# Kernel optimization log

Measured on AMD Instinct MI355X. Metric: run time of the kernel, lower is better.

Reference implementation:

```python
import jax, jax.numpy as jnp
import numpy as np
import math

B, T, C = 2, 1024, 1024
H = 16
HS = C // H          # head size 64
ROT = HS // 2        # rotary dims 32
TT = 1024            # ctx_len
FFN = 4 * C
EPS = 1e-6


def _layernorm(x, g, b):
    m = jnp.mean(x, -1, keepdims=True)
    v = jnp.mean((x - m) ** 2, -1, keepdims=True)
    return (x - m) * jax.lax.rsqrt(v + EPS) * g + b


def _time_shift_half(x):
    # ZeroPad2d((0,0,1,-1)) applied to first half of channels: shift by one step in time
    c = x.shape[-1]
    a = jnp.pad(x[:, :, : c // 2], ((0, 0), (1, 0), (0, 0)))[:, :-1, :]
    return jnp.concatenate([a, x[:, :, c // 2 :]], axis=-1)


def _rotate_half(x):
    x1, x2 = jnp.split(x, 2, axis=-1)
    return jnp.concatenate([-x2, x1], axis=-1)


def _rotary_cos_sin(t_len, rot, base):
    inv_freq = 1.0 / (base ** (jnp.arange(0, rot, 2, dtype=jnp.float32) / rot))
    freqs = jnp.arange(t_len, dtype=jnp.float32)[:, None] * inv_freq[None, :]
    emb = jnp.concatenate([freqs, freqs], axis=-1)  # (T, rot)
    return jnp.cos(emb), jnp.sin(emb)


def _build_w(time_w, time_alpha, time_beta, t_len):
    # faithful translation of the pad/tile/reshape circulant trick
    w = jnp.pad(time_w, ((0, 0), (0, TT)))            # (H, 2TT)
    w = jnp.tile(w, (1, TT))                          # (H, 2TT*TT)
    w = w[:, :-TT].reshape(-1, TT, 2 * TT - 1)        # (H, TT, 2TT-1)
    w = w[:, :, TT - 1 :]                             # (H, TT, TT)
    return w[:, :t_len, :t_len] * time_alpha[:, :, :t_len] * time_beta[:, :t_len, :]


def setup_inputs() -> dict:
    key = jax.random.key(0)
    ks = jax.random.split(key, 24)
    s = 0.02
    d = {
        "x": jax.random.normal(ks[0], (B, T, C), jnp.float32),
        "ln1_g": jnp.ones((C,), jnp.float32),
        "ln1_b": jnp.zeros((C,), jnp.float32),
        "Wq": jax.random.normal(ks[1], (C, C), jnp.float32) * s,
        "bq": jnp.zeros((C,), jnp.float32),
        "Wk": jax.random.normal(ks[2], (C, C), jnp.float32) * s,
        "bk": jnp.zeros((C,), jnp.float32),
        "Wv": jax.random.normal(ks[3], (C, C), jnp.float32) * s,
        "bv": jnp.zeros((C,), jnp.float32),
        "Wo": jax.random.normal(ks[4], (C, C), jnp.float32) * s,
        "bo": jnp.zeros((C,), jnp.float32),
        "time_w": 1.0 + 0.01 * jax.random.normal(ks[5], (H, TT), jnp.float32),
        "time_alpha": 1.0 + 0.01 * jax.random.normal(ks[6], (H, 1, TT), jnp.float32),
        "time_beta": 1.0 + 0.01 * jax.random.normal(ks[7], (H, TT, 1), jnp.float32),
        "time_gamma": 1.0 + 0.01 * jax.random.normal(ks[8], (TT, 1), jnp.float32),
        "Wmix": jnp.eye(H, dtype=jnp.float32) + 0.01 * jax.random.normal(ks[9], (H, H), jnp.float32),
        "ln2_g": jnp.ones((C,), jnp.float32),
        "ln2_b": jnp.zeros((C,), jnp.float32),
        "Wgk": jax.random.normal(ks[10], (C, FFN), jnp.float32) * s,
        "bgk": jnp.zeros((FFN,), jnp.float32),
        "Wgv": jax.random.normal(ks[11], (C, FFN), jnp.float32) * s,
        "bgv": jnp.zeros((FFN,), jnp.float32),
        "Wgw": jax.random.normal(ks[12], (FFN, C), jnp.float32) * s,
        "bgw": jnp.zeros((C,), jnp.float32),
    }
    return d


def _block(x, ln1_g, ln1_b, Wq, bq, Wk, bk, Wv, bv, Wo, bo,
           time_w, time_alpha, time_beta, time_gamma, Wmix,
           ln2_g, ln2_b, Wgk, bgk, Wgv, bgv, Wgw, bgw):
    b, t, c = x.shape
    # ---- MHA_pro attention sublayer (pre-LN residual) ----
    xs = _time_shift_half(_layernorm(x, ln1_g, ln1_b))
    q = (xs @ Wq + bq).reshape(b, t, H, HS).transpose(0, 2, 1, 3)  # bhtd
    k = (xs @ Wk + bk).reshape(b, t, H, HS).transpose(0, 2, 1, 3)
    v = (xs @ Wv + bv).reshape(b, t, H, HS).transpose(0, 2, 1, 3)
    qr, qp = q[..., :ROT], q[..., ROT:]
    kr, kp = k[..., :ROT], k[..., ROT:]
    cos, sin = _rotary_cos_sin(t, ROT, float(TT))  # base = ctx_len
    qr = qr * cos + _rotate_half(qr) * sin
    kr = kr * cos + _rotate_half(kr) * sin
    q = jnp.concatenate([qr, qp], axis=-1)
    k = jnp.concatenate([kr, kp], axis=-1)
    att = jnp.einsum("bhtd,bhud->bhtu", q, k) * (1.0 / math.sqrt(HS))
    causal = jnp.tril(jnp.ones((t, t), bool))
    att = jnp.where(causal, att, -jnp.inf)
    att = jax.nn.softmax(att, axis=-1)
    w = _build_w(time_w, time_alpha, time_beta, t)  # (H, T, T)
    att = att * w[None]
    att = jnp.einsum("ij,bjtu->bitu", Wmix, att)  # 1x1 conv head mix
    y = jnp.einsum("bhtu,bhud->bhtd", att, v)
    y = y.transpose(0, 2, 1, 3).reshape(b, t, c)
    y = (y @ Wo + bo) * time_gamma[:t, :]
    x = x + y
    # ---- GeGLU MLP sublayer (pre-LN residual) ----
    xm = _layernorm(x, ln2_g, ln2_b)
    kk = xm @ Wgk + bgk
    vv = xm @ Wgv + bgv
    y2 = (jax.nn.gelu(kk, approximate=False) * vv) @ Wgw + bgw
    return x + y2


def reference(x, ln1_g, ln1_b, Wq, bq, Wk, bk, Wv, bv, Wo, bo,
              time_w, time_alpha, time_beta, time_gamma, Wmix,
              ln2_g, ln2_b, Wgk, bgk, Wgv, bgv, Wgw, bgw):
    return _block(x, ln1_g, ln1_b, Wq, bq, Wk, bk, Wv, bv, Wo, bo,
                  time_w, time_alpha, time_beta, time_gamma, Wmix,
                  ln2_g, ln2_b, Wgk, bgk, Wgv, bgv, Wgw, bgw)
```

## Files before the change

### kernel.cpp

```cpp
#include <hip/hip_runtime.h>
#include <math.h>

typedef unsigned short u16;
typedef short s16x8 __attribute__((ext_vector_type(8)));
typedef float f32x4 __attribute__((ext_vector_type(4)));

#define TB 2
#define TSEQ 1024
#define CC 1024
#define NH 16
#define HSZ 64
#define FFN 4096
#define MROWS (TB*TSEQ)

#define GLOAD16(g, l) __builtin_amdgcn_global_load_lds( \
    (const __attribute__((address_space(1))) unsigned*)(g), \
    (__attribute__((address_space(3))) unsigned*)(l), 16, 0, 0)

#define SBAR()  __builtin_amdgcn_s_barrier()
#define SCHED0() __builtin_amdgcn_sched_barrier(0)
#define LGKM0() asm volatile("s_waitcnt lgkmcnt(0)" ::: "memory")
#define WAITV4() asm volatile("s_waitcnt vmcnt(4)" ::: "memory")
#define PRIO(n) __builtin_amdgcn_s_setprio(n)

__device__ __forceinline__ float bf2f(u16 u){
  union { unsigned u; float f; } c; c.u = ((unsigned)u) << 16; return c.f;
}
__device__ __forceinline__ u16 f2bf(float f){
  union { float f; unsigned u; } c; c.f = f;
  unsigned u = c.u;
  u += 0x7fffu + ((u >> 16) & 1);
  return (u16)(u >> 16);
}
__device__ __forceinline__ float ldin(const void* p, size_t i, int bf){
  return bf ? bf2f(((const u16*)p)[i]) : ((const float*)p)[i];
}

__global__ void k_flag(const unsigned* __restrict__ g, int* __restrict__ flag){
  if (threadIdx.x == 0) *flag = (g[0] == 0x3F800000u) ? 0 : 1;
}

__global__ void k_transpose_cvt(const void* __restrict__ in, u16* __restrict__ out,
                                int R, int Cc, const int* __restrict__ flagp){
  int bf = *flagp;
  __shared__ u16 tile[32][33];
  int bx = blockIdx.x * 32, by = blockIdx.y * 32;
  int tx = threadIdx.x & 31, ty = threadIdx.x >> 5;
  #pragma unroll
  for (int i = 0; i < 32; i += 8)
    tile[ty + i][tx] = f2bf(ldin(in, (size_t)(by + ty + i) * Cc + bx + tx, bf));
  __syncthreads();
  #pragma unroll
  for (int i = 0; i < 32; i += 8)
    out[(size_t)(bx + ty + i) * R + by + tx] = tile[tx][ty + i];
}

__global__ void k_cvt(const void* __restrict__ in, u16* __restrict__ out, int n,
                      const int* __restrict__ flagp){
  int bf = *flagp;
  int i = blockIdx.x * 256 + threadIdx.x;
  if (i < n) out[i] = f2bf(ldin(in, i, bf));
}

__global__ void k_tw8(const void* __restrict__ tw, u16* __restrict__ tw8,
                      const int* __restrict__ flagp){
  int bf = *flagp;
  int idx = blockIdx.x*256 + threadIdx.x;
  int s = idx >> 14;
  int h = (idx >> 10) & 15;
  int k = idx & 1023;
  float v = (k + s < 1024) ? ldin(tw, h*1024 + k + s, bf) : 0.f;
  tw8[idx] = f2bf(v);
}

__global__ void k_ln1_shift(const void* __restrict__ x, const void* __restrict__ g,
                            const void* __restrict__ bta, u16* __restrict__ xs,
                            const int* __restrict__ flagp){
  int bf = *flagp;
  int row = blockIdx.x;
  int t = row & (TSEQ - 1);
  int tid = threadIdx.x;
  float v[4]; float s = 0.f, ss = 0.f;
  #pragma unroll
  for (int i = 0; i < 4; i++){
    v[i] = ldin(x, (size_t)row * CC + tid*4 + i, bf);
    s += v[i]; ss += v[i]*v[i];
  }
  __shared__ float rs[256], rss[256];
  rs[tid] = s; rss[tid] = ss; __syncthreads();
  for (int o = 128; o > 0; o >>= 1){ if (tid < o){ rs[tid] += rs[tid+o]; rss[tid] += rss[tid+o]; } __syncthreads(); }
  float mean = rs[0] * (1.0f/CC);
  float var  = rss[0] * (1.0f/CC) - mean*mean;
  float inv  = rsqrtf(var + 1e-6f);
  #pragma unroll
  for (int i = 0; i < 4; i++){
    int c = tid*4 + i;
    float o = (v[i]-mean)*inv*ldin(g, c, bf) + ldin(bta, c, bf);
    u16 ob = f2bf(o);
    if (c >= CC/2)            xs[(size_t)row*CC + c] = ob;
    else if (t < TSEQ-1)      xs[(size_t)(row+1)*CC + c] = ob;
  }
  if (t == 0 && tid < 128){
    #pragma unroll
    for (int i = 0; i < 4; i++) xs[(size_t)row*CC + tid*4 + i] = 0;
  }
}

__global__ void k_ln2(const float* __restrict__ x1, const void* __restrict__ g,
                      const void* __restrict__ bta, u16* __restrict__ xm,
                      const int* __restrict__ flagp){
  int bf = *flagp;
  int row = blockIdx.x;
  int tid = threadIdx.x;
  const float* xr = x1 + (size_t)row * CC;
  float v[4]; float s = 0.f, ss = 0.f;
  #pragma unroll
  for (int i = 0; i < 4; i++){ v[i] = xr[tid*4 + i]; s += v[i]; ss += v[i]*v[i]; }
  __shared__ float rs[256], rss[256];
  rs[tid] = s; rss[tid] = ss; __syncthreads();
  for (int o = 128; o > 0; o >>= 1){ if (tid < o){ rs[tid] += rs[tid+o]; rss[tid] += rss[tid+o]; } __syncthreads(); }
  float mean = rs[0] * (1.0f/CC);
  float var  = rss[0] * (1.0f/CC) - mean*mean;
  float inv  = rsqrtf(var + 1e-6f);
  #pragma unroll
  for (int i = 0; i < 4; i++){
    int c = tid*4 + i;
    xm[(size_t)row*CC + c] = f2bf((v[i]-mean)*inv*ldin(g, c, bf) + ldin(bta, c, bf));
  }
}

__global__ void k_rotary(u16* __restrict__ qkv){
  int idx = blockIdx.x*256 + threadIdx.x;
  int i = idx & 15;
  int h = (idx >> 4) & (NH-1);
  int row = idx >> 8;
  int t = row & (TSEQ-1);
  float invf = exp2f(-0.625f * (float)i);
  float ang = (float)t * invf;
  float cs = cosf(ang), sn = sinf(ang);
  size_t base = (size_t)row * (3*CC);
  u16* qp = qkv + base + h*HSZ;
  float a = bf2f(qp[i]), b2 = bf2f(qp[i+16]);
  qp[i]    = f2bf(a*cs - b2*sn);
  qp[i+16] = f2bf(b2*cs + a*sn);
  u16* kp = qkv + base + CC + h*HSZ;
  a = bf2f(kp[i]); b2 = bf2f(kp[i+16]);
  kp[i]    = f2bf(a*cs - b2*sn);
  kp[i+16] = f2bf(b2*cs + a*sn);
}

__global__ __launch_bounds__(256) void k_qk(
    const u16* __restrict__ qkv, u16* __restrict__ att)
{
  int m0 = blockIdx.y * 128;
  int n0 = blockIdx.x * 128;
  if (n0 > m0) return;
  int bh = blockIdx.z; int b = bh >> 4, h = bh & 15;
  __shared__ u16 As[128*32];
  __shared__ u16 Bs[128*32];
  int tid = threadIdx.x;
  int w = tid >> 6;
  int lane = tid & 63;
  int wm = (w >> 1) * 64, wn = (w & 1) * 64;
  f32x4 acc[4][4];
  #pragma unroll
  for (int i = 0; i < 4; i++)
    #pragma unroll
    for (int j = 0; j < 4; j++) acc[i][j] = (f32x4){0.f,0.f,0.f,0.f};

  int rr = lane >> 2;
  int cc = lane & 3;
  const u16* gA0 = qkv + (size_t)(b*TSEQ + m0 + w*32 + rr)*(3*CC) + h*HSZ + cc*8;
  const u16* gA1 = gA0 + (size_t)16*(3*CC);
  const u16* gB0 = qkv + (size_t)(b*TSEQ + n0 + w*32 + rr)*(3*CC) + CC + h*HSZ + cc*8;
  const u16* gB1 = gB0 + (size_t)16*(3*CC);
  u16* lA0 = As + (w*32)*32;
  u16* lA1 = As + (w*32+16)*32;
  u16* lB0 = Bs + (w*32)*32;
  u16* lB1 = Bs + (w*32+16)*32;
  int quad = lane >> 4;
  int l15 = lane & 15;

  #pragma unroll
  for (int k0 = 0; k0 < HSZ; k0 += 32){
    __syncthreads();
    GLOAD16(gA0 + k0, lA0);
    GLOAD16(gA1 + k0, lA1);
    GLOAD16(gB0 + k0, lB0);
    GLOAD16(gB1 + k0, lB1);
    __syncthreads();
    s16x8 af[4], bfr[4];
    #pragma unroll
    for (int i = 0; i < 4; i++){
      af[i]  = *(s16x8*)&As[(wm + i*16 + l15)*32 + quad*8];
      bfr[i] = *(s16x8*)&Bs[(wn + i*16 + l15)*32 + quad*8];
    }
    #pragma unroll
    for (int mi = 0; mi < 4; mi++)
      #pragma unroll
      for (int ni = 0; ni < 4; ni++)
        acc[mi][ni] = __builtin_amdgcn_mfma_f32_16x16x32_bf16(af[mi], bfr[ni], acc[mi][ni], 0, 0, 0);
  }

  #pragma unroll
  for (int mi = 0; mi < 4; mi++){
    int rowb = m0 + wm + mi*16 + quad*4;
    #pragma unroll
    for (int ni = 0; ni < 4; ni++){
      int col = n0 + wn + ni*16 + l15;
      #pragma unroll
      for (int r = 0; r < 4; r++){
        int t = rowb + r;
        att[((size_t)bh*TSEQ + t)*TSEQ + col] = f2bf(acc[mi][ni][r] * 0.125f);
      }
    }
  }
}

__global__ __launch_bounds__(256) void k_softmix(
    u16* __restrict__ att, const u16* __restrict__ tw8, const u16* __restrict__ al16,
    const u16* __restrict__ be16, const void* __restrict__ wmix,
    const int* __restrict__ flagp)
{
  int bf = *flagp;
  int bt = blockIdx.x;
  int t = bt & (TSEQ-1);
  int b = bt >> 10;
  int tid = threadIdx.x;
  int wv = tid >> 6;
  int lane = tid & 63;
  int tile_end = ((t >> 7) + 1) << 7;
  int nchunk = (t >> 9) + 1;
  int sh = (TSEQ-1 - t) & 7;
  int base = (TSEQ-1 - t) - sh;
  __shared__ __align__(16) u16 P[NH][TSEQ];
  __shared__ float wm[NH*NH];
  if (tid < NH*NH) wm[tid] = ldin(wmix, tid, bf);

  #pragma unroll
  for (int hi = 0; hi < 4; hi++){
    int h = wv*4 + hi;
    const u16* srow = att + ((size_t)(b*NH + h)*TSEQ + t)*TSEQ;
    const u16* twp  = tw8 + ((size_t)sh*NH + h)*TSEQ + base;
    const u16* alp  = al16 + h*TSEQ;
    float v[16];
    float lmax = -1e30f;
    for (int r = 0; r < nchunk; r++){
      int ub = lane*8 + r*512;
      uint4 pk = *(const uint4*)(srow + ub);
      const u16* pe = (const u16*)&pk;
      #pragma unroll
      for (int e = 0; e < 8; e++){
        float s = bf2f(pe[e]);
        if (ub + e > t) s = -1e30f;
        v[r*8+e] = s;
        lmax = fmaxf(lmax, s);
      }
    }
    #pragma unroll
    for (int o = 32; o > 0; o >>= 1) lmax = fmaxf(lmax, __shfl_xor(lmax, o));
    float lsum = 0.f;
    for (int r = 0; r < nchunk; r++){
      #pragma unroll
      for (int e = 0; e < 8; e++){
        float p = __expf(v[r*8+e] - lmax);
        v[r*8+e] = p; lsum += p;
      }
    }
    #pragma unroll
    for (int o = 32; o > 0; o >>= 1) lsum += __shfl_xor(lsum, o);
    float btv = bf2f(be16[h*TSEQ + t]);
    float inv = btv / lsum;
    for (int r = 0; r < nchunk; r++){
      int ub = lane*8 + r*512;
      uint4 wk = *(const uint4*)(twp + ub);
      uint4 ak = *(const uint4*)(alp + ub);
      const u16* we = (const u16*)&wk;
      const u16* ae = (const u16*)&ak;
      u16 tmp[8];
      #pragma unroll
      for (int e = 0; e < 8; e++){
        float p = v[r*8+e] * inv * bf2f(we[e]) * bf2f(ae[e]);
        tmp[e] = f2bf(p);
      }
      *(uint4*)&P[h][ub] = *(uint4*)tmp;
    }
  }
  __syncthreads();

  int u0 = tid * 4;
  if (u0 < tile_end){
    #pragma unroll
    for (int half2 = 0; half2 < 2; half2++){
      float acc[8][4];
      #pragma unroll
      for (int i = 0; i < 8; i++)
        #pragma unroll
        for (int k = 0; k < 4; k++) acc[i][k] = 0.f;
      #pragma unroll
      for (int j = 0; j < 16; j++){
        uint2 pk = *(const uint2*)&P[j][u0];
        float p0 = bf2f((u16)(pk.x & 0xffff)), p1 = bf2f((u16)(pk.x >> 16));
        float p2 = bf2f((u16)(pk.y & 0xffff)), p3 = bf2f((u16)(pk.y >> 16));
        #pragma unroll
        for (int i2 = 0; i2 < 8; i2++){
          float w = wm[(half2*8 + i2)*NH + j];
          acc[i2][0] += w*p0; acc[i2][1] += w*p1; acc[i2][2] += w*p2; acc[i2][3] += w*p3;
        }
      }
      #pragma unroll
      for (int i2 = 0; i2 < 8; i2++){
        int i = half2*8 + i2;
        u16 tmp[4] = {f2bf(acc[i2][0]), f2bf(acc[i2][1]), f2bf(acc[i2][2]), f2bf(acc[i2][3])};
        *(uint2*)(att + ((size_t)(b*NH + i)*TSEQ + t)*TSEQ + u0) = *(uint2*)tmp;
      }
    }
  }
}

__global__ void k_vt(const u16* __restrict__ qkv, u16* __restrict__ vt){
  __shared__ u16 tile[32][33];
  int bh = blockIdx.z; int b = bh >> 4, h = bh & 15;
  int u0 = blockIdx.x * 32, d0 = blockIdx.y * 32;
  int tx = threadIdx.x & 31, ty = threadIdx.x >> 5;
  #pragma unroll
  for (int i = 0; i < 32; i += 8)
    tile[ty + i][tx] = qkv[(size_t)(b*TSEQ + u0 + ty + i)*(3*CC) + 2*CC + h*HSZ + d0 + tx];
  __syncthreads();
  #pragma unroll
  for (int i = 0; i < 32; i += 8)
    vt[((size_t)bh*HSZ + d0 + ty + i)*TSEQ + u0 + tx] = tile[tx][ty + i];
}

__global__ void k_gelumul(const u16* __restrict__ kkvv, u16* __restrict__ hh){
  int idx = blockIdx.x*256 + threadIdx.x;
  int m = idx >> 9;
  int j = (idx & 511) * 8;
  uint4 kk4 = *(const uint4*)(kkvv + (size_t)m*(2*FFN) + j);
  uint4 vv4 = *(const uint4*)(kkvv + (size_t)m*(2*FFN) + FFN + j);
  const u16* ks = (const u16*)&kk4;
  const u16* vs = (const u16*)&vv4;
  u16 out[8];
  #pragma unroll
  for (int e = 0; e < 8; e++){
    float kk = bf2f(ks[e]), vv = bf2f(vs[e]);
    float ge = 0.5f*kk*(1.0f + erff(kk*0.70710678f));
    out[e] = f2bf(ge*vv);
  }
  *(uint4*)(hh + (size_t)m*FFN + j) = *(uint4*)out;
}

__global__ __launch_bounds__(512, 2) void k_gemm256(
    const u16* __restrict__ A, const u16* __restrict__ Bt,
    const u16* __restrict__ bias, int M, int N, int K, int mode,
    u16* __restrict__ outp, float* __restrict__ partial)
{
  __shared__ u16 S[65536];
  u16* SA0 = S;
  u16* SB0 = S + 16384;
  u16* SA1 = S + 32768;
  u16* SB1 = S + 49152;

  int nwg = (int)(gridDim.x * gridDim.y * gridDim.z);
  int lin = (int)(blockIdx.x + gridDim.x * (blockIdx.y + gridDim.y * blockIdx.z));
  int nl  = (nwg & 7) ? lin : ((lin & 7) * (nwg >> 3) + (lin >> 3));
  int bx  = nl % (int)gridDim.x;
  int tq  = nl / (int)gridDim.x;
  int by  = tq % (int)gridDim.y;
  int bz  = tq / (int)gridDim.y;

  int m0 = by * 256, n0 = bx * 256;
  int kper = K / (int)gridDim.z;
  int kbeg = bz * kper;
  int nt = kper >> 6;
  int niter = nt >> 1;

  int tid = threadIdx.x;
  int w = tid >> 6, lane = tid & 63;
  int wm = w >> 2, wn = w & 3;
  int quad = lane >> 4, l15 = lane & 15;
  int l3 = lane >> 3, ch = (lane & 7) ^ l3;

  const u16* gA = A  + (size_t)(m0 + w*16 + l3) * K + ch*8 + kbeg;
  const u16* gB = Bt + (size_t)(n0 + w*16 + l3) * K + ch*8 + kbeg;
  const size_t hstep = (size_t)128 * K;
  const size_t rstep = (size_t)8 * K;

  int pc0 = quad ^ (l15 & 7);
  int pc1 = (4 + quad) ^ (l15 & 7);
  int aoff0 = (wm*128 + l15)*64 + pc0*8;
  int aoff1 = (wm*128 + l15)*64 + pc1*8;
  int boff0 = (wn*64 + l15)*64 + pc0*8;
  int boff1 = (wn*64 + l15)*64 + pc1*8;

  f32x4 acc[8][4];
  #pragma unroll
  for (int i = 0; i < 8; i++)
    #pragma unroll
    for (int j = 0; j < 4; j++) acc[i][j] = (f32x4){0.f,0.f,0.f,0.f};

  #define STG(gbase, sbase, h, ko) do{ \
      const u16* _g = (gbase) + (size_t)(h)*hstep + (ko); \
      u16* _l = (sbase) + ((h)*128 + w*16)*64; \
      GLOAD16(_g, _l); \
      GLOAD16(_g + rstep, _l + 512); \
    }while(0)

  #define LD_A(buf, MQ) do{ _Pragma("unroll") for (int _m = 0; _m < 4; _m++){ \
      a0[_m] = *(const s16x8*)((buf) + aoff0 + (MQ)*4096 + _m*1024); \
      a1[_m] = *(const s16x8*)((buf) + aoff1 + (MQ)*4096 + _m*1024); } }while(0)

  #define LD_B(buf, NQ, B0A, B1A) do{ _Pragma("unroll") for (int _n = 0; _n < 2; _n++){ \
      B0A[_n] = *(const s16x8*)((buf) + boff0 + (NQ)*2048 + _n*1024); \
      B1A[_n] = *(const s16x8*)((buf) + boff1 + (NQ)*2048 + _n*1024); } }while(0)

  #define MMQ(MQ, NQ, B0A, B1A) do{ _Pragma("unroll") for (int _m = 0; _m < 4; _m++){ \
      _Pragma("unroll") for (int _n = 0; _n < 2; _n++){ \
        acc[(MQ)*4+_m][(NQ)*2+_n] = __builtin_amdgcn_mfma_f32_16x16x32_bf16(a0[_m], B0A[_n], acc[(MQ)*4+_m][(NQ)*2+_n], 0, 0, 0); \
        acc[(MQ)*4+_m][(NQ)*2+_n] = __builtin_amdgcn_mfma_f32_16x16x32_bf16(a1[_m], B1A[_n], acc[(MQ)*4+_m][(NQ)*2+_n], 0, 0, 0); }} }while(0)

  STG(gB, SB0, 0, 0); STG(gB, SB0, 1, 0);
  STG(gA, SA0, 0, 0); STG(gA, SA0, 1, 0);
  STG(gB, SB1, 0, 64); STG(gB, SB1, 1, 64);
  WAITV4();
  SBAR();

  s16x8 a0[4], a1[4], bl0[2], bl1[2], bh0[2], bh1[2];

  for (int i = 0; i < niter; i++){
    int t1k = (2*i+1)*64;
    int t2k = (2*i+2 < nt) ? (2*i+2)*64 : 0;
    int t3k = (2*i+3 < nt) ? (2*i+3)*64 : 0;

    LD_A(SA0, 0); LD_B(SB0, 0, bl0, bl1);
    STG(gA, SA1, 0, t1k);
    SBAR(); LGKM0(); SCHED0(); PRIO(1); MMQ(0,0,bl0,bl1); PRIO(0); SBAR();
    LD_B(SB0, 1, bh0, bh1);
    STG(gA, SA1, 1, t1k);
    SBAR(); LGKM0(); SCHED0(); PRIO(1); MMQ(0,1,bh0,bh1); PRIO(0); SBAR();
    LD_A(SA0, 1);
    STG(gB, SB0, 0, t2k);
    SBAR(); LGKM0(); SCHED0(); PRIO(1); MMQ(1,0,bl0,bl1); PRIO(0); SBAR();
    STG(gB, SB0, 1, t2k);
    SBAR(); LGKM0(); SCHED0(); PRIO(1); MMQ(1,1,bh0,bh1); PRIO(0);
    WAITV4(); SBAR();
    LD_A(SA1, 0); LD_B(SB1, 0, bl0, bl1);
    STG(gA, SA0, 0, t2k);
    SBAR(); LGKM0(); SCHED0(); PRIO(1); MMQ(0,0,bl0,bl1); PRIO(0); SBAR();
    LD_B(SB1, 1, bh0, bh1);
    STG(gA, SA0, 1, t2k);
    SBAR(); LGKM0(); SCHED0(); PRIO(1); MMQ(0,1,bh0,bh1); PRIO(0); SBAR();
    LD_A(SA1, 1);
    STG(gB, SB1, 0, t3k);
    SBAR(); LGKM0(); SCHED0(); PRIO(1); MMQ(1,0,bl0,bl1); PRIO(0); SBAR();
    STG(gB, SB1, 1, t3k);
    SBAR(); LGKM0(); SCHED0(); PRIO(1); MMQ(1,1,bh0,bh1); PRIO(0);
    WAITV4(); SBAR();
  }

  if (mode == 3){
    float* pout = partial + (size_t)bz * M * N;
    #pragma unroll
    for (int mi = 0; mi < 8; mi++){
      int rowb = m0 + wm*128 + mi*16 + quad*4;
      #pragma unroll
      for (int ni = 0; ni < 4; ni++){
        int col = n0 + wn*64 + ni*16 + l15;
        #pragma unroll
        for (int r = 0; r < 4; r++)
          pout[(size_t)(rowb + r) * N + col] = acc[mi][ni][r];
      }
    }
  } else {
    #pragma unroll
    for (int mi = 0; mi < 8; mi++){
      int rowb = m0 + wm*128 + mi*16 + quad*4;
      #pragma unroll
      for (int ni = 0; ni < 4; ni++){
        int col = n0 + wn*64 + ni*16 + l15;
        float bv = bf2f(bias[col]);
        #pragma unroll
        for (int r = 0; r < 4; r++)
          outp[(size_t)(rowb + r) * N + col] = f2bf(acc[mi][ni][r] + bv);
      }
    }
  }
  #undef STG
  #undef LD_A
  #undef LD_B
  #undef MMQ
}

__global__ __launch_bounds__(256) void k_gemm(
    const u16* __restrict__ A, const u16* __restrict__ Bt,
    const u16* __restrict__ bias, int M, int N, int K, int mode,
    void* __restrict__ outp, const void* __restrict__ xres,
    const float* __restrict__ resf, const u16* __restrict__ gamma,
    float* __restrict__ partial, const int* __restrict__ flagp)
{
  int bf = *flagp;
  __shared__ u16 As[128*32];
  __shared__ u16 Bs[128*32];
  int tid = threadIdx.x;
  int m0 = blockIdx.y * 128;
  int n0 = blockIdx.x * 128;
  int nz = gridDim.z;
  int kper = K / nz;
  int kbeg = blockIdx.z * kper;
  int kend = kbeg + kper;
  int w = tid >> 6;
  int lane = tid & 63;
  int wm = (w >> 1) * 64, wn = (w & 1) * 64;
  f32x4 acc[4][4];
  #pragma unroll
  for (int i = 0; i < 4; i++)
    #pragma unroll
    for (int j = 0; j < 4; j++) acc[i][j] = (f32x4){0.f,0.f,0.f,0.f};

  int rr = lane >> 2;
  int cc = lane & 3;
  const u16* gA0 = A  + (size_t)(m0 + w*32 + rr)*K + cc*8;
  const u16* gA1 = gA0 + (size_t)16*K;
  const u16* gB0 = Bt + (size_t)(n0 + w*32 + rr)*K + cc*8;
  const u16* gB1 = gB0 + (size_t)16*K;
  u16* lA0 = As + (w*32)*32;
  u16* lA1 = As + (w*32+16)*32;
  u16* lB0 = Bs + (w*32)*32;
  u16* lB1 = Bs + (w*32+16)*32;
  int quad = lane >> 4;
  int l15 = lane & 15;

  for (int k0 = kbeg; k0 < kend; k0 += 32){
    __syncthreads();
    GLOAD16(gA0 + k0, lA0);
    GLOAD16(gA1 + k0, lA1);
    GLOAD16(gB0 + k0, lB0);
    GLOAD16(gB1 + k0, lB1);
    __syncthreads();
    s16x8 af[4], bfr[4];
    #pragma unroll
    for (int i = 0; i < 4; i++){
      af[i]  = *(s16x8*)&As[(wm + i*16 + l15)*32 + quad*8];
      bfr[i] = *(s16x8*)&Bs[(wn + i*16 + l15)*32 + quad*8];
    }
    #pragma unroll
    for (int mi = 0; mi < 4; mi++)
      #pragma unroll
      for (int ni = 0; ni < 4; ni++)
        acc[mi][ni] = __builtin_amdgcn_mfma_f32_16x16x32_bf16(af[mi], bfr[ni], acc[mi][ni], 0, 0, 0);
  }

  if (nz > 1){
    float* pout = partial + (size_t)blockIdx.z * M * N;
    #pragma unroll
    for (int mi = 0; mi < 4; mi++){
      int rowb = m0 + wm + mi*16 + quad*4;
      #pragma unroll
      for (int ni = 0; ni < 4; ni++){
        int col = n0 + wn + ni*16 + l15;
        #pragma unroll
        for (int r = 0; r < 4; r++)
          pout[(size_t)(rowb + r) * N + col] = acc[mi][ni][r];
      }
    }
    return;
  }

  #pragma unroll
  for (int mi = 0; mi < 4; mi++){
    int rowb = m0 + wm + mi*16 + quad*4;
    #pragma unroll
    for (int ni = 0; ni < 4; ni++){
      int col = n0 + wn + ni*16 + l15;
      float bv = bf2f(bias[col]);
      #pragma unroll
      for (int r = 0; r < 4; r++){
        int row = rowb + r;
        float val = acc[mi][ni][r] + bv;
        size_t idx = (size_t)row * N + col;
        if (mode == 0){
          ((u16*)outp)[idx] = f2bf(val);
        } else if (mode == 1){
          int t = row & (TSEQ-1);
          ((float*)outp)[idx] = ldin(xres, idx, bf) + val * bf2f(gamma[t]);
        } else {
          float o = resf[idx] + val;
          if (bf) ((u16*)outp)[idx] = f2bf(o);
          else    ((float*)outp)[idx] = o;
        }
      }
    }
  }
}

__global__ void k_reduceK(const float* __restrict__ partial, int nsplit,
                          int M, int N, const u16* __restrict__ bias, int mode,
                          void* __restrict__ outp, const void* __restrict__ xres,
                          const float* __restrict__ resf, const u16* __restrict__ gamma,
                          const int* __restrict__ flagp){
  int bf = *flagp;
  int idx = blockIdx.x*256 + threadIdx.x;
  int row = idx / (N/4);
  int c0  = (idx % (N/4)) * 4;
  size_t base = (size_t)row * N + c0;
  float v[4] = {0.f, 0.f, 0.f, 0.f};
  for (int s = 0; s < nsplit; s++){
    const float4 p = *(const float4*)(partial + (size_t)s * M * N + base);
    v[0] += p.x; v[1] += p.y; v[2] += p.z; v[3] += p.w;
  }
  #pragma unroll
  for (int e = 0; e < 4; e++) v[e] += bf2f(bias[c0 + e]);
  if (mode == 1){
    int t = row & (TSEQ-1);
    float gm = bf2f(gamma[t]);
    float o[4];
    #pragma unroll
    for (int e = 0; e < 4; e++) o[e] = ldin(xres, base + e, bf) + v[e] * gm;
    *(float4*)((float*)outp + base) = (float4){o[0], o[1], o[2], o[3]};
  } else {
    float o[4];
    #pragma unroll
    for (int e = 0; e < 4; e++) o[e] = resf[base + e] + v[e];
    if (bf){
      u16 tmp[4] = {f2bf(o[0]), f2bf(o[1]), f2bf(o[2]), f2bf(o[3])};
      *(uint2*)((u16*)outp + base) = *(uint2*)tmp;
    } else {
      *(float4*)((float*)outp + base) = (float4){o[0], o[1], o[2], o[3]};
    }
  }
}

__global__ __launch_bounds__(256) void k_pv(
    const u16* __restrict__ att, const u16* __restrict__ vt, u16* __restrict__ y)
{
  __shared__ u16 As[128*32];
  __shared__ u16 Bs[64*32];
  int tid = threadIdx.x;
  int bh = blockIdx.y; int b = bh >> 4, h = bh & 15;
  int m0 = blockIdx.x * 128;
  const u16* A  = att + (size_t)bh * TSEQ * TSEQ;
  const u16* Bt = vt  + (size_t)bh * HSZ * TSEQ;
  int w = tid >> 6;
  int lane = tid & 63;
  int wm = (w >> 1) * 64, wn = (w & 1) * 32;
  f32x4 acc[4][2];
  #pragma unroll
  for (int i = 0; i < 4; i++){ acc[i][0] = (f32x4){0,0,0,0}; acc[i][1] = (f32x4){0,0,0,0}; }

  int rr = lane >> 2;
  int cc = lane & 3;
  const u16* gA0 = A + (size_t)(m0 + w*32 + rr)*TSEQ + cc*8;
  const u16* gA1 = gA0 + (size_t)16*TSEQ;
  const u16* gB0 = Bt + (size_t)(w*16 + rr)*TSEQ + cc*8;
  u16* lA0 = As + (w*32)*32;
  u16* lA1 = As + (w*32+16)*32;
  u16* lB0 = Bs + (w*16)*32;
  int quad = lane >> 4;
  int l15 = lane & 15;
  int kend = m0 + 128;

  for (int k0 = 0; k0 < kend; k0 += 32){
    __syncthreads();
    GLOAD16(gA0 + k0, lA0);
    GLOAD16(gA1 + k0, lA1);
    GLOAD16(gB0 + k0, lB0);
    __syncthreads();
    s16x8 af[4], bfr[2];
    #pragma unroll
    for (int i = 0; i < 4; i++)
      af[i] = *(s16x8*)&As[(wm + i*16 + l15)*32 + quad*8];
    #pragma unroll
    for (int i = 0; i < 2; i++)
      bfr[i] = *(s16x8*)&Bs[(wn + i*16 + l15)*32 + quad*8];
    #pragma unroll
    for (int mi = 0; mi < 4; mi++)
      #pragma unroll
      for (int ni = 0; ni < 2; ni++)
        acc[mi][ni] = __builtin_amdgcn_mfma_f32_16x16x32_bf16(af[mi], bfr[ni], acc[mi][ni], 0, 0, 0);
  }

  #pragma unroll
  for (int mi = 0; mi < 4; mi++){
    int rowb = m0 + wm + mi*16 + quad*4;
    #pragma unroll
    for (int ni = 0; ni < 2; ni++){
      int col = wn + ni*16 + l15;
      #pragma unroll
      for (int r = 0; r < 4; r++){
        int t = rowb + r;
        y[(size_t)(b*TSEQ + t)*CC + h*HSZ + col] = f2bf(acc[mi][ni][r]);
      }
    }
  }
}

extern "C" void kernel_launch(void* const* d_in, const int* in_sizes, int n_in,
                              void* d_out, int out_size, void* d_ws, size_t ws_size,
                              hipStream_t stream){
  const void* x     = d_in[0];
  const void* ln1g  = d_in[1];
  const void* ln1b  = d_in[2];
  const void* Wq    = d_in[3];
  const void* bq    = d_in[4];
  const void* Wk    = d_in[5];
  const void* bk    = d_in[6];
  const void* Wv    = d_in[7];
  const void* bv    = d_in[8];
  const void* Wo    = d_in[9];
  const void* bo    = d_in[10];
  const void* timew = d_in[11];
  const void* alpha = d_in[12];
  const void* beta  = d_in[13];
  const void* gamma = d_in[14];
  const void* Wmix  = d_in[15];
  const void* ln2g  = d_in[16];
  const void* ln2b  = d_in[17];
  const void* Wgk   = d_in[18];
  const void* bgk   = d_in[19];
  const void* Wgv   = d_in[20];
  const void* bgv   = d_in[21];
  const void* Wgw   = d_in[22];
  const void* bgw   = d_in[23];

  char* ws = (char*)d_ws;
  size_t off = 0;
  auto carve = [&](size_t bytes)->char*{
    char* p = ws + off; off = (off + bytes + 255) & ~(size_t)255; return p;
  };
  int*  FLAG   = (int*)carve(256);
  u16*  WT_QKV = (u16*)carve(3072ull*1024*2);
  u16*  WT_O   = (u16*)carve(1024ull*1024*2);
  u16*  WT_G   = (u16*)carve(8192ull*1024*2);
  u16*  WT_W   = (u16*)carve(1024ull*4096*2);
  u16*  B_QKV  = (u16*)carve(3072*2);
  u16*  B_G    = (u16*)carve(8192*2);
  u16*  B_O    = (u16*)carve(1024*2);
  u16*  B_W    = (u16*)carve(1024*2);
  u16*  GMA    = (u16*)carve(1024*2);
  u16*  TW8    = (u16*)carve(8ull*16*1024*2 + 4096);
  u16*  AL16   = (u16*)carve(16*1024*2);
  u16*  BE16   = (u16*)carve(16*1024*2);
  u16*  XS     = (u16*)carve((size_t)MROWS*CC*2);
  u16*  QKV    = (u16*)carve((size_t)MROWS*3*CC*2);
  u16*  ATT    = (u16*)carve((size_t)TB*NH*TSEQ*TSEQ*2);
  u16*  VT     = (u16*)carve((size_t)TB*NH*HSZ*TSEQ*2);
  u16*  Y      = (u16*)carve((size_t)MROWS*CC*2);
  float* X1    = (float*)carve((size_t)MROWS*CC*4);
  u16*  XM     = (u16*)carve((size_t)MROWS*CC*2);
  u16*  KKVV   = (u16*)carve((size_t)MROWS*2*FFN*2);
  u16*  HH     = (u16*)carve((size_t)MROWS*FFN*2);
  float* PART  = (float*)ATT;
  (void)ws_size; (void)in_sizes; (void)n_in; (void)out_size;

  k_flag<<<1,64,0,stream>>>((const unsigned*)ln1g, FLAG);

  k_transpose_cvt<<<dim3(32,32),256,0,stream>>>(Wq, WT_QKV,                1024, 1024, FLAG);
  k_transpose_cvt<<<dim3(32,32),256,0,stream>>>(Wk, WT_QKV + 1024*1024,    1024, 1024, FLAG);
  k_transpose_cvt<<<dim3(32,32),256,0,stream>>>(Wv, WT_QKV + 2*1024*1024,  1024, 1024, FLAG);
  k_transpose_cvt<<<dim3(32,32),256,0,stream>>>(Wo, WT_O,                  1024, 1024, FLAG);
  k_transpose_cvt<<<dim3(128,32),256,0,stream>>>(Wgk, WT_G,                1024, 4096, FLAG);
  k_transpose_cvt<<<dim3(128,32),256,0,stream>>>(Wgv, WT_G + 4096ull*1024, 1024, 4096, FLAG);
  k_transpose_cvt<<<dim3(32,128),256,0,stream>>>(Wgw, WT_W,                4096, 1024, FLAG);
  k_cvt<<<4,256,0,stream>>>(bq, B_QKV,        1024, FLAG);
  k_cvt<<<4,256,0,stream>>>(bk, B_QKV + 1024, 1024, FLAG);
  k_cvt<<<4,256,0,stream>>>(bv, B_QKV + 2048, 1024, FLAG);
  k_cvt<<<16,256,0,stream>>>(bgk, B_G,        4096, FLAG);
  k_cvt<<<16,256,0,stream>>>(bgv, B_G + 4096, 4096, FLAG);
  k_cvt<<<4,256,0,stream>>>(bo,  B_O, 1024, FLAG);
  k_cvt<<<4,256,0,stream>>>(bgw, B_W, 1024, FLAG);
  k_cvt<<<4,256,0,stream>>>(gamma, GMA, 1024, FLAG);
  k_tw8<<<512,256,0,stream>>>(timew, TW8, FLAG);
  k_cvt<<<64,256,0,stream>>>(alpha, AL16, 16384, FLAG);
  k_cvt<<<64,256,0,stream>>>(beta,  BE16, 16384, FLAG);

  k_ln1_shift<<<MROWS,256,0,stream>>>(x, ln1g, ln1b, XS, FLAG);
  k_gemm256<<<dim3(12,8),512,0,stream>>>(XS, WT_QKV, B_QKV, MROWS, 3072, 1024, 0,
                                         QKV, nullptr);
  k_rotary<<<2048,256,0,stream>>>(QKV);
  k_qk<<<dim3(8,8,TB*NH),256,0,stream>>>(QKV, ATT);
  k_softmix<<<TB*TSEQ,256,0,stream>>>(ATT, TW8, AL16, BE16, Wmix, FLAG);
  k_vt<<<dim3(32,2,32),256,0,stream>>>(QKV, VT);
  k_pv<<<dim3(8,32),256,0,stream>>>(ATT, VT, Y);

  k_gemm<<<dim3(8,16,2),256,0,stream>>>(Y, WT_O, B_O, MROWS, 1024, 1024, 1,
                                        nullptr, nullptr, nullptr, nullptr, PART, FLAG);
  k_reduceK<<<MROWS*1024/(4*256),256,0,stream>>>(PART, 2, MROWS, 1024, B_O, 1,
                                                 X1, x, nullptr, GMA, FLAG);

  k_ln2<<<MROWS,256,0,stream>>>(X1, ln2g, ln2b, XM, FLAG);
  k_gemm256<<<dim3(32,8),512,0,stream>>>(XM, WT_G, B_G, MROWS, 8192, 1024, 0,
                                         KKVV, nullptr);
  k_gelumul<<<(MROWS*FFN)/(256*8),256,0,stream>>>(KKVV, HH);

  k_gemm256<<<dim3(4,8,8),512,0,stream>>>(HH, WT_W, nullptr, MROWS, 1024, 4096, 3,
                                          nullptr, PART);
  k_reduceK<<<MROWS*1024/(4*256),256,0,stream>>>(PART, 8, MROWS, 1024, B_W, 2,
                                                 d_out, nullptr, X1, nullptr, FLAG);
}
```

Measured before the change: 440.8 us.

## Batch prep launches into fused kernels, warp-shuffle LN reductions, precomputed rotary table

```diff
diff --git a/kernel.cpp b/kernel.cpp
--- a/kernel.cpp
+++ b/kernel.cpp
@@ -40,37 +40,58 @@
   if (threadIdx.x == 0) *flag = (g[0] == 0x3F800000u) ? 0 : 1;
 }
 
-__global__ void k_transpose_cvt(const void* __restrict__ in, u16* __restrict__ out,
-                                int R, int Cc, const int* __restrict__ flagp){
+struct Prep {
+  const void* csrc[10]; u16* cdst[10]; int cp0[11];
+  const void* tw; u16* tw8; float2* rt;
+};
+__global__ void k_prep(Prep P, const int* __restrict__ flagp){
+  int bf = *flagp;
+  int blk = blockIdx.x, tid = threadIdx.x;
+  if (blk < 184){
+    int idx = blk*256 + tid;
+    int s = 0;
+    #pragma unroll
+    for (int i = 1; i < 10; i++) if (idx >= P.cp0[i]) s = i;
+    int r = idx - P.cp0[s];
+    P.cdst[s][r] = f2bf(ldin(P.csrc[s], r, bf));
+  } else if (blk < 696){
+    int idx = (blk-184)*256 + tid;
+    int s = idx >> 14;
+    int h = (idx >> 10) & 15;
+    int k = idx & 1023;
+    float v = (k + s < 1024) ? ldin(P.tw, h*1024 + k + s, bf) : 0.f;
+    P.tw8[idx] = f2bf(v);
+  } else {
+    int idx = (blk-696)*256 + tid;
+    int i = idx & 15, t = idx >> 4;
+    float invf = exp2f(-0.625f * (float)i);
+    float ang = (float)t * invf;
+    P.rt[idx] = (float2){cosf(ang), sinf(ang)};
+  }
+}
+
+struct TEnt { const void* src; u16* dst; int R, C, bxn, blk0; };
+struct TPack { TEnt e[7]; };
+__global__ void k_transpose_all(TPack p, const int* __restrict__ flagp){
   int bf = *flagp;
   __shared__ u16 tile[32][33];
-  int bx = blockIdx.x * 32, by = blockIdx.y * 32;
+  int blk = blockIdx.x;
+  int ei = 0;
+  #pragma unroll
+  for (int i = 1; i < 7; i++) if (blk >= p.e[i].blk0) ei = i;
+  const void* src = p.e[ei].src;
+  u16* dst = p.e[ei].dst;
+  int R = p.e[ei].R, C = p.e[ei].C;
+  int rel = blk - p.e[ei].blk0;
+  int bx = (rel % p.e[ei].bxn) * 32, by = (rel / p.e[ei].bxn) * 32;
   int tx = threadIdx.x & 31, ty = threadIdx.x >> 5;
   #pragma unroll
   for (int i = 0; i < 32; i += 8)
-    tile[ty + i][tx] = f2bf(ldin(in, (size_t)(by + ty + i) * Cc + bx + tx, bf));
+    tile[ty + i][tx] = f2bf(ldin(src, (size_t)(by + ty + i) * C + bx + tx, bf));
   __syncthreads();
   #pragma unroll
   for (int i = 0; i < 32; i += 8)
-    out[(size_t)(bx + ty + i) * R + by + tx] = tile[tx][ty + i];
-}
-
-__global__ void k_cvt(const void* __restrict__ in, u16* __restrict__ out, int n,
-                      const int* __restrict__ flagp){
-  int bf = *flagp;
-  int i = blockIdx.x * 256 + threadIdx.x;
-  if (i < n) out[i] = f2bf(ldin(in, i, bf));
-}
-
-__global__ void k_tw8(const void* __restrict__ tw, u16* __restrict__ tw8,
-                      const int* __restrict__ flagp){
-  int bf = *flagp;
-  int idx = blockIdx.x*256 + threadIdx.x;
-  int s = idx >> 14;
-  int h = (idx >> 10) & 15;
-  int k = idx & 1023;
-  float v = (k + s < 1024) ? ldin(tw, h*1024 + k + s, bf) : 0.f;
-  tw8[idx] = f2bf(v);
+    dst[(size_t)(bx + ty + i) * R + by + tx] = tile[tx][ty + i];
 }
 
 __global__ void k_ln1_shift(const void* __restrict__ x, const void* __restrict__ g,
@@ -80,17 +101,22 @@
   int row = blockIdx.x;
   int t = row & (TSEQ - 1);
   int tid = threadIdx.x;
+  int wv = tid >> 6, lane = tid & 63;
   float v[4]; float s = 0.f, ss = 0.f;
   #pragma unroll
   for (int i = 0; i < 4; i++){
     v[i] = ldin(x, (size_t)row * CC + tid*4 + i, bf);
     s += v[i]; ss += v[i]*v[i];
   }
-  __shared__ float rs[256], rss[256];
-  rs[tid] = s; rss[tid] = ss; __syncthreads();
-  for (int o = 128; o > 0; o >>= 1){ if (tid < o){ rs[tid] += rs[tid+o]; rss[tid] += rss[tid+o]; } __syncthreads(); }
-  float mean = rs[0] * (1.0f/CC);
-  float var  = rss[0] * (1.0f/CC) - mean*mean;
+  #pragma unroll
+  for (int o = 32; o > 0; o >>= 1){ s += __shfl_xor(s, o); ss += __shfl_xor(ss, o); }
+  __shared__ float rs[4], rss[4];
+  if (lane == 0){ rs[wv] = s; rss[wv] = ss; }
+  __syncthreads();
+  float S = rs[0]+rs[1]+rs[2]+rs[3];
+  float SS = rss[0]+rss[1]+rss[2]+rss[3];
+  float mean = S * (1.0f/CC);
+  float var  = SS * (1.0f/CC) - mean*mean;
   float inv  = rsqrtf(var + 1e-6f);
   #pragma unroll
   for (int i = 0; i < 4; i++){
@@ -112,15 +138,20 @@
   int bf = *flagp;
   int row = blockIdx.x;
   int tid = threadIdx.x;
+  int wv = tid >> 6, lane = tid & 63;
   const float* xr = x1 + (size_t)row * CC;
   float v[4]; float s = 0.f, ss = 0.f;
   #pragma unroll
   for (int i = 0; i < 4; i++){ v[i] = xr[tid*4 + i]; s += v[i]; ss += v[i]*v[i]; }
-  __shared__ float rs[256], rss[256];
-  rs[tid] = s; rss[tid] = ss; __syncthreads();
-  for (int o = 128; o > 0; o >>= 1){ if (tid < o){ rs[tid] += rs[tid+o]; rss[tid] += rss[tid+o]; } __syncthreads(); }
-  float mean = rs[0] * (1.0f/CC);
-  float var  = rss[0] * (1.0f/CC) - mean*mean;
+  #pragma unroll
+  for (int o = 32; o > 0; o >>= 1){ s += __shfl_xor(s, o); ss += __shfl_xor(ss, o); }
+  __shared__ float rs[4], rss[4];
+  if (lane == 0){ rs[wv] = s; rss[wv] = ss; }
+  __syncthreads();
+  float S = rs[0]+rs[1]+rs[2]+rs[3];
+  float SS = rss[0]+rss[1]+rss[2]+rss[3];
+  float mean = S * (1.0f/CC);
+  float var  = SS * (1.0f/CC) - mean*mean;
   float inv  = rsqrtf(var + 1e-6f);
   #pragma unroll
   for (int i = 0; i < 4; i++){
@@ -129,15 +160,14 @@
   }
 }
 
-__global__ void k_rotary(u16* __restrict__ qkv){
+__global__ void k_rotary(u16* __restrict__ qkv, const float2* __restrict__ rt){
   int idx = blockIdx.x*256 + threadIdx.x;
   int i = idx & 15;
   int h = (idx >> 4) & (NH-1);
   int row = idx >> 8;
   int t = row & (TSEQ-1);
-  float invf = exp2f(-0.625f * (float)i);
-  float ang = (float)t * invf;
-  float cs = cosf(ang), sn = sinf(ang);
+  float2 cssn = rt[t*16 + i];
+  float cs = cssn.x, sn = cssn.y;
   size_t base = (size_t)row * (3*CC);
   u16* qp = qkv + base + h*HSZ;
   float a = bf2f(qp[i]), b2 = bf2f(qp[i+16]);
@@ -749,34 +779,44 @@
   u16*  XM     = (u16*)carve((size_t)MROWS*CC*2);
   u16*  KKVV   = (u16*)carve((size_t)MROWS*2*FFN*2);
   u16*  HH     = (u16*)carve((size_t)MROWS*FFN*2);
+  float2* RT   = (float2*)carve((size_t)TSEQ*16*8);
   float* PART  = (float*)ATT;
   (void)ws_size; (void)in_sizes; (void)n_in; (void)out_size;
 
   k_flag<<<1,64,0,stream>>>((const unsigned*)ln1g, FLAG);
 
-  k_transpose_cvt<<<dim3(32,32),256,0,stream>>>(Wq, WT_QKV,                1024, 1024, FLAG);
-  k_transpose_cvt<<<dim3(32,32),256,0,stream>>>(Wk, WT_QKV + 1024*1024,    1024, 1024, FLAG);
-  k_transpose_cvt<<<dim3(32,32),256,0,stream>>>(Wv, WT_QKV + 2*1024*1024,  1024, 1024, FLAG);
-  k_transpose_cvt<<<dim3(32,32),256,0,stream>>>(Wo, WT_O,                  1024, 1024, FLAG);
-  k_transpose_cvt<<<dim3(128,32),256,0,stream>>>(Wgk, WT_G,                1024, 4096, FLAG);
-  k_transpose_cvt<<<dim3(128,32),256,0,stream>>>(Wgv, WT_G + 4096ull*1024, 1024, 4096, FLAG);
-  k_transpose_cvt<<<dim3(32,128),256,0,stream>>>(Wgw, WT_W,                4096, 1024, FLAG);
-  k_cvt<<<4,256,0,stream>>>(bq, B_QKV,        1024, FLAG);
-  k_cvt<<<4,256,0,stream>>>(bk, B_QKV + 1024, 1024, FLAG);
-  k_cvt<<<4,256,0,stream>>>(bv, B_QKV + 2048, 1024, FLAG);
-  k_cvt<<<16,256,0,stream>>>(bgk, B_G,        4096, FLAG);
-  k_cvt<<<16,256,0,stream>>>(bgv, B_G + 4096, 4096, FLAG);
-  k_cvt<<<4,256,0,stream>>>(bo,  B_O, 1024, FLAG);
-  k_cvt<<<4,256,0,stream>>>(bgw, B_W, 1024, FLAG);
-  k_cvt<<<4,256,0,stream>>>(gamma, GMA, 1024, FLAG);
-  k_tw8<<<512,256,0,stream>>>(timew, TW8, FLAG);
-  k_cvt<<<64,256,0,stream>>>(alpha, AL16, 16384, FLAG);
-  k_cvt<<<64,256,0,stream>>>(beta,  BE16, 16384, FLAG);
+  Prep P;
+  P.csrc[0]=bq;    P.cdst[0]=B_QKV;
+  P.csrc[1]=bk;    P.cdst[1]=B_QKV+1024;
+  P.csrc[2]=bv;    P.cdst[2]=B_QKV+2048;
+  P.csrc[3]=bgk;   P.cdst[3]=B_G;
+  P.csrc[4]=bgv;   P.cdst[4]=B_G+4096;
+  P.csrc[5]=bo;    P.cdst[5]=B_O;
+  P.csrc[6]=bgw;   P.cdst[6]=B_W;
+  P.csrc[7]=gamma; P.cdst[7]=GMA;
+  P.csrc[8]=alpha; P.cdst[8]=AL16;
+  P.csrc[9]=beta;  P.cdst[9]=BE16;
+  int sizes[10] = {1024,1024,1024,4096,4096,1024,1024,1024,16384,16384};
+  int acc0 = 0;
+  for (int i = 0; i < 10; i++){ P.cp0[i] = acc0; acc0 += sizes[i]; }
+  P.cp0[10] = acc0;
+  P.tw = timew; P.tw8 = TW8; P.rt = RT;
+  k_prep<<<760,256,0,stream>>>(P, FLAG);
+
+  TPack T;
+  T.e[0] = {Wq,  WT_QKV,                1024, 1024,  32,     0};
+  T.e[1] = {Wk,  WT_QKV + 1024*1024,    1024, 1024,  32,  1024};
+  T.e[2] = {Wv,  WT_QKV + 2*1024*1024,  1024, 1024,  32,  2048};
+  T.e[3] = {Wo,  WT_O,                  1024, 1024,  32,  3072};
+  T.e[4] = {Wgk, WT_G,                  1024, 4096, 128,  4096};
+  T.e[5] = {Wgv, WT_G + 4096ull*1024,   1024, 4096, 128,  8192};
+  T.e[6] = {Wgw, WT_W,                  4096, 1024,  32, 12288};
+  k_transpose_all<<<16384,256,0,stream>>>(T, FLAG);
 
   k_ln1_shift<<<MROWS,256,0,stream>>>(x, ln1g, ln1b, XS, FLAG);
   k_gemm256<<<dim3(12,8),512,0,stream>>>(XS, WT_QKV, B_QKV, MROWS, 3072, 1024, 0,
                                          QKV, nullptr);
-  k_rotary<<<2048,256,0,stream>>>(QKV);
+  k_rotary<<<2048,256,0,stream>>>(QKV, RT);
   k_qk<<<dim3(8,8,TB*NH),256,0,stream>>>(QKV, ATT);
   k_softmix<<<TB*TSEQ,256,0,stream>>>(ATT, TW8, AL16, BE16, Wmix, FLAG);
   k_vt<<<dim3(32,2,32),256,0,stream>>>(QKV, VT);
```

After: 406.8 us. 7.7% less time.
